# Kernel tuning notes

Measured on AMD Instinct MI355X. Metric: run time of the kernel, lower is better.

The kernel has to match this reference:

```python
import jax, jax.numpy as jnp
import numpy as np

NL, H, N, CIN, COUT, B, L = 4, 256, 64, 64, 8, 8, 1024
LN_EPS = 1e-5


def layernorm(x, w, b):
    m = x.mean(-1, keepdims=True)
    v = ((x - m) ** 2).mean(-1, keepdims=True)
    return (x - m) / jnp.sqrt(v + LN_EPS) * w + b


def s4d(u, A, C, D, log_step):
    # u: [B, H, L] real; A: [N] complex; C: [H, N] complex
    Lq = u.shape[-1]
    step = jnp.exp(log_step)                       # [H]
    dA = step[:, None] * A[None, :]                # [H, N] complex
    C_bar = C * (jnp.exp(dA) - 1.0) / A[None, :]   # [H, N]
    l = jnp.arange(Lq, dtype=jnp.float32)
    P = jnp.exp(l[:, None, None] * dA[None])       # [L, H, N] complex (dominant intermediate)
    K = jnp.einsum('hn,lhn->hl', C_bar, P)         # [H, L] complex
    kf = jnp.fft.rfft(K.real, n=2 * Lq) + 1j * jnp.fft.rfft(K.imag, n=2 * Lq)  # [H, L+1]
    uf = jnp.fft.rfft(u, n=2 * Lq)                 # [B, H, L+1]
    y = jnp.fft.irfft(kf * uf, n=2 * Lq)[..., :Lq]  # [B, H, L] real
    return y + u * D[:, None]


def forward(stimulus_seq, initial_state, A_re, A_im, C_re, C_im, D, log_step,
            ln1_w, ln1_b, ln2_w, ln2_b, W1, b1, W2, b2,
            Win, b_in, Wst, b_st, Wout, b_out):
    # stimulus_seq: [B, CIN, L] -> [B, L, CIN]
    x = stimulus_seq.transpose(0, 2, 1) @ Win.T + b_in            # [B, L, H]
    x = x + (initial_state @ Wst.T + b_st)[:, None, :]            # fusion_mode='add'
    for i in range(NL):
        xn = layernorm(x, ln1_w[i], ln1_b[i])
        A = A_re[i] + 1j * A_im[i]
        C = C_re[i] + 1j * C_im[i]
        y = s4d(xn.transpose(0, 2, 1), A, C, D[i], log_step[i])
        x = x + y.transpose(0, 2, 1)
        xn = layernorm(x, ln2_w[i], ln2_b[i])
        h = jax.nn.gelu(xn @ W1[i].T + b1[i], approximate=False)  # torch GELU = exact erf
        x = x + h @ W2[i].T + b2[i]
    out = x @ Wout.T + b_out                                      # [B, L, COUT]
    # use_voltage_filter=False: split + concat is identity on channel axis
    return out.transpose(0, 2, 1)                                 # [B, COUT, L]


def setup_inputs() -> dict:
    key = jax.random.key(0)
    ks = iter(jax.random.split(key, 24))
    def u(shape, fan_in):
        lim = 1.0 / np.sqrt(fan_in)
        return jax.random.uniform(next(ks), shape, minval=-lim, maxval=lim, dtype=jnp.float32)
    inp = {
        'stimulus_seq': jax.random.normal(next(ks), (B, CIN, L), dtype=jnp.float32),
        'initial_state': jax.random.normal(next(ks), (B, COUT), dtype=jnp.float32),
        'A_re': -0.5 * jnp.ones((NL, N), dtype=jnp.float32),
        'A_im': jnp.tile(jnp.arange(N, dtype=jnp.float32) * np.float32(np.pi), (NL, 1)),
        'C_re': jax.random.normal(next(ks), (NL, H, N), dtype=jnp.float32),
        'C_im': jax.random.normal(next(ks), (NL, H, N), dtype=jnp.float32),
        'D': jax.random.normal(next(ks), (NL, H), dtype=jnp.float32),
        'log_step': jax.random.uniform(next(ks), (NL, H), dtype=jnp.float32) * np.float32(np.log(0.1) - np.log(1e-4)) + np.float32(np.log(1e-4)),
        'ln1_w': jnp.ones((NL, H), dtype=jnp.float32),
        'ln1_b': jnp.zeros((NL, H), dtype=jnp.float32),
        'ln2_w': jnp.ones((NL, H), dtype=jnp.float32),
        'ln2_b': jnp.zeros((NL, H), dtype=jnp.float32),
        'W1': u((NL, 2 * H, H), H), 'b1': u((NL, 2 * H), H),
        'W2': u((NL, H, 2 * H), 2 * H), 'b2': u((NL, H), 2 * H),
        'Win': u((H, CIN), CIN), 'b_in': u((H,), CIN),
        'Wst': u((H, COUT), COUT), 'b_st': u((H,), COUT),
        'Wout': u((COUT, H), H), 'b_out': u((COUT,), H),
    }
    return inp


def reference(stimulus_seq, initial_state, A_re, A_im, C_re, C_im, D, log_step,
              ln1_w, ln1_b, ln2_w, ln2_b, W1, b1, W2, b2,
              Win, b_in, Wst, b_st, Wout, b_out):
    return forward(stimulus_seq, initial_state, A_re, A_im, C_re, C_im, D, log_step,
                   ln1_w, ln1_b, ln2_w, ln2_b, W1, b1, W2, b2,
                   Win, b_in, Wst, b_st, Wout, b_out)
```

## Files before the change

### kernel.cpp

```cpp
#include <hip/hip_runtime.h>
#include <math.h>

#define NL   4
#define H    256
#define NST  64
#define CIN  64
#define COUT 8
#define BB   8
#define LL   1024
#define NFFT 2048

typedef __attribute__((ext_vector_type(8))) short bf16x8;
typedef __attribute__((ext_vector_type(4))) short short4v;
typedef __attribute__((ext_vector_type(4))) int   int4v;
typedef __attribute__((ext_vector_type(4))) float f32x4;

__device__ __forceinline__ short f2bf(float f) {
  union { float f; unsigned u; } v; v.f = f;
  unsigned r = (v.u + 0x7fffu + ((v.u >> 16) & 1u)) >> 16;
  return (short)r;
}
__device__ __forceinline__ float b2f(short s) {
  union { unsigned u; float f; } v;
  v.u = ((unsigned)(unsigned short)s) << 16;
  return v.f;
}
__device__ __forceinline__ int IDX2(int a) { return a + (a >> 4); }
#define FBUF 2176

__device__ __forceinline__ float2 cadd(float2 a, float2 b) { return make_float2(a.x + b.x, a.y + b.y); }
__device__ __forceinline__ float2 csub(float2 a, float2 b) { return make_float2(a.x - b.x, a.y - b.y); }

template <int SGN>
__device__ __forceinline__ void bfly8(const float2 a[8], float2 A[8]) {
  const float RH = 0.70710678118654752f;
  float2 s0 = cadd(a[0], a[4]), s1 = csub(a[0], a[4]);
  float2 s2 = cadd(a[2], a[6]), s3 = csub(a[2], a[6]);
  float2 mi = (SGN < 0) ? make_float2(s3.y, -s3.x) : make_float2(-s3.y, s3.x);
  float2 E0 = cadd(s0, s2), E1 = cadd(s1, mi), E2 = csub(s0, s2), E3 = csub(s1, mi);
  float2 t0 = cadd(a[1], a[5]), t1 = csub(a[1], a[5]);
  float2 t2 = cadd(a[3], a[7]), t3 = csub(a[3], a[7]);
  float2 mj = (SGN < 0) ? make_float2(t3.y, -t3.x) : make_float2(-t3.y, t3.x);
  float2 O0 = cadd(t0, t2), O1 = cadd(t1, mj), O2 = csub(t0, t2), O3 = csub(t1, mj);
  float2 W0 = O0;
  float2 W1 = (SGN < 0) ? make_float2((O1.x + O1.y) * RH, (O1.y - O1.x) * RH)
                        : make_float2((O1.x - O1.y) * RH, (O1.x + O1.y) * RH);
  float2 W2 = (SGN < 0) ? make_float2(O2.y, -O2.x) : make_float2(-O2.y, O2.x);
  float2 W3 = (SGN < 0) ? make_float2((O3.y - O3.x) * RH, -(O3.x + O3.y) * RH)
                        : make_float2(-(O3.x + O3.y) * RH, (O3.x - O3.y) * RH);
  A[0] = cadd(E0, W0); A[4] = csub(E0, W0);
  A[1] = cadd(E1, W1); A[5] = csub(E1, W1);
  A[2] = cadd(E2, W2); A[6] = csub(E2, W2);
  A[3] = cadd(E3, W3); A[7] = csub(E3, W3);
}

template <int SGN>
__device__ __forceinline__ void fft_stage0_reg(const float2 a[8], float2* d,
                                               const float2* __restrict__ tw, int tid) {
  float2 A[8];
  bfly8<SGN>(a, A);
  const int base = 8 * tid;
  d[IDX2(base)] = A[0];
#pragma unroll
  for (int dd = 1; dd < 8; ++dd) {
    float2 w = tw[dd * tid];
    float wi = (SGN < 0) ? w.y : -w.y;
    d[IDX2(base + dd)] = make_float2(A[dd].x * w.x - A[dd].y * wi,
                                     A[dd].x * wi + A[dd].y * w.x);
  }
}

template <int SGN>
__device__ __forceinline__ void fft_stage0_reg_tw(const float2 a[8], float2* d,
                                                  const float2 w[7], int tid) {
  float2 A[8];
  bfly8<SGN>(a, A);
  const int base = 8 * tid;
  d[IDX2(base)] = A[0];
#pragma unroll
  for (int dd = 1; dd < 8; ++dd) {
    float wr = w[dd - 1].x;
    float wi = (SGN < 0) ? w[dd - 1].y : -w[dd - 1].y;
    d[IDX2(base + dd)] = make_float2(A[dd].x * wr - A[dd].y * wi,
                                     A[dd].x * wi + A[dd].y * wr);
  }
}

template <int SGN>
__device__ __forceinline__ void fft_mid_stages(float2* bA, float2* bB,
                                               const float2* __restrict__ tw, int tid) {
#pragma unroll
  for (int st = 1; st < 3; ++st) {
    float2* s = (st == 1) ? bA : bB;
    float2* d = (st == 1) ? bB : bA;
    const int m = 1 << (3 * st);
    __syncthreads();
    const int k  = tid & (m - 1);
    const int jm = tid - k;
    float2 a[8], A[8];
#pragma unroll
    for (int q = 0; q < 8; ++q) a[q] = s[IDX2(tid + 256 * q)];
    bfly8<SGN>(a, A);
    const int base = 8 * jm + k;
    d[IDX2(base)] = A[0];
#pragma unroll
    for (int dd = 1; dd < 8; ++dd) {
      float2 w = tw[dd * jm];
      float wi = (SGN < 0) ? w.y : -w.y;
      d[IDX2(base + dd * m)] = make_float2(A[dd].x * w.x - A[dd].y * wi,
                                           A[dd].x * wi + A[dd].y * w.x);
    }
  }
}

template <int SGN>
__device__ __forceinline__ void fft_final_r4_lds(const float2* s, float2* d, int tid) {
  __syncthreads();
#pragma unroll
  for (int q = 0; q < 2; ++q) {
    const int t = tid + (q << 8);
    float2 x0 = s[IDX2(t)], x1 = s[IDX2(t + 512)];
    float2 x2 = s[IDX2(t + 1024)], x3 = s[IDX2(t + 1536)];
    float2 s0 = cadd(x0, x2), s1 = csub(x0, x2);
    float2 s2 = cadd(x1, x3), s3 = csub(x1, x3);
    float2 mi = (SGN < 0) ? make_float2(s3.y, -s3.x) : make_float2(-s3.y, s3.x);
    d[IDX2(t)]        = cadd(s0, s2);
    d[IDX2(t + 512)]  = cadd(s1, mi);
    d[IDX2(t + 1024)] = csub(s0, s2);
    d[IDX2(t + 1536)] = csub(s1, mi);
  }
  __syncthreads();
}

template <int SGN>
__device__ __forceinline__ void fft_final_r4_reg(const float2* s, int tid,
                                                 float2 out0[4], float2 out1[4]) {
  __syncthreads();
#pragma unroll
  for (int q = 0; q < 2; ++q) {
    const int t = tid + (q << 8);
    float2 x0 = s[IDX2(t)], x1 = s[IDX2(t + 512)];
    float2 x2 = s[IDX2(t + 1024)], x3 = s[IDX2(t + 1536)];
    float2 s0 = cadd(x0, x2), s1 = csub(x0, x2);
    float2 s2 = cadd(x1, x3), s3 = csub(x1, x3);
    float2 mi = (SGN < 0) ? make_float2(s3.y, -s3.x) : make_float2(-s3.y, s3.x);
    float2* o = q ? out1 : out0;
    o[0] = cadd(s0, s2);
    o[1] = cadd(s1, mi);
    o[2] = csub(s0, s2);
    o[3] = csub(s1, mi);
  }
}

__global__ __launch_bounds__(256) void k_setup(
    const float* __restrict__ W1, const float* __restrict__ W2, const float* __restrict__ Win,
    const float* __restrict__ init, const float* __restrict__ Wst,
    const float* __restrict__ bst, const float* __restrict__ bin,
    short* __restrict__ W1s, short* __restrict__ W2s, float* __restrict__ WinT,
    float* __restrict__ sp, float2* __restrict__ tw) {
  int idx = blockIdx.x * 256 + threadIdx.x;
  if (idx < 2048) {
    float s, c;
    sincosf(3.14159265358979323846f * (float)idx / 1024.0f, &s, &c);
    tw[idx] = make_float2(c, -s);
  }
  if (idx < 65536) {
    int i = idx >> 14, c = idx & 16383;
    int cblk = c >> 11, s = (c >> 8) & 7, n = (c >> 6) & 3, lane = c & 63;
    int cl = lane & 15, rg = lane >> 4;
    int col = cblk * 64 + n * 16 + cl;
    const float* srcp = W1 + ((size_t)(i * 512 + col)) * 256 + s * 32 + rg * 8;
    short* dstp = W1s + ((size_t)idx) * 8;
#pragma unroll
    for (int j = 0; j < 8; ++j) dstp[j] = f2bf(srcp[j]);
  } else if (idx < 131072) {
    int t = idx - 65536;
    int i = t >> 14, c = t & 16383;
    int cblk = c >> 11, s = (c >> 7) & 15, n = (c >> 6) & 1, lane = c & 63;
    int cl = lane & 15, rg = lane >> 4;
    int col = cblk * 32 + n * 16 + cl;
    const float* srcp = W2 + ((size_t)(i * 256 + col)) * 512 + s * 32 + rg * 8;
    short* dstp = W2s + ((size_t)t) * 8;
#pragma unroll
    for (int j = 0; j < 8; ++j) dstp[j] = f2bf(srcp[j]);
  }
  if (idx < 256 * 64) {
    int hh = idx / 64, c = idx % 64;
    WinT[c * 256 + hh] = Win[idx];
  }
  if (idx < BB * H) {
    int b = idx >> 8, h = idx & 255;
    float acc = bin[h] + bst[h];
#pragma unroll
    for (int c = 0; c < COUT; ++c) acc += init[b * COUT + c] * Wst[h * COUT + c];
    sp[idx] = acc;
  }
}

__global__ __launch_bounds__(256) void k_in_ln1(
    const float* __restrict__ stim, const float* __restrict__ WinT,
    const float* __restrict__ sp, const float* __restrict__ lw, const float* __restrict__ lb,
    short* __restrict__ x, float* __restrict__ xnT) {
  int blk = blockIdx.x;
  int b_ = blk >> 6, l0 = (blk & 63) << 4;
  int tid = threadIdx.x, wv = tid >> 6, lane = tid & 63;
  __shared__ float sc[16][CIN];
  __shared__ float T[16][256];
#pragma unroll
  for (int it = 0; it < 4; ++it) {
    int idx = tid + (it << 8);
    int r = idx & 15, c = idx >> 4;
    sc[r][c] = stim[(b_ * CIN + c) * LL + l0 + r];
  }
  __syncthreads();
  float4 sp4 = *(const float4*)&sp[b_ * H + lane * 4];
  float4 acc[4] = {sp4, sp4, sp4, sp4};
  for (int c = 0; c < CIN; ++c) {
    float4 wv4 = *(const float4*)&WinT[c * H + lane * 4];
#pragma unroll
    for (int rr = 0; rr < 4; ++rr) {
      float s = sc[wv * 4 + rr][c];
      acc[rr].x += s * wv4.x; acc[rr].y += s * wv4.y;
      acc[rr].z += s * wv4.z; acc[rr].w += s * wv4.w;
    }
  }
  float4 w4 = *(const float4*)&lw[lane * 4];
  float4 c4 = *(const float4*)&lb[lane * 4];
#pragma unroll
  for (int rr = 0; rr < 4; ++rr) {
    int lr = wv * 4 + rr;
    float4 v = acc[rr];
    short4v s4;
    s4[0] = f2bf(v.x); s4[1] = f2bf(v.y); s4[2] = f2bf(v.z); s4[3] = f2bf(v.w);
    *(short4v*)&x[(((size_t)(b_ << 10) + l0 + lr)) * H + lane * 4] = s4;
    float s = v.x + v.y + v.z + v.w;
#pragma unroll
    for (int o = 32; o > 0; o >>= 1) s += __shfl_xor(s, o, 64);
    float m = s * (1.0f / H);
    float dx = v.x - m, dy = v.y - m, dz = v.z - m, dw = v.w - m;
    float q = dx * dx + dy * dy + dz * dz + dw * dw;
#pragma unroll
    for (int o = 32; o > 0; o >>= 1) q += __shfl_xor(q, o, 64);
    float rs = rsqrtf(q * (1.0f / H) + 1e-5f);
    float4 o4;
    o4.x = dx * rs * w4.x + c4.x; o4.y = dy * rs * w4.y + c4.y;
    o4.z = dz * rs * w4.z + c4.z; o4.w = dw * rs * w4.w + c4.w;
    *(float4*)&T[lr][lane * 4] = o4;
  }
  __syncthreads();
  float tmp[16];
#pragma unroll
  for (int l = 0; l < 16; ++l) tmp[l] = T[l][tid];
  float* dst = xnT + ((size_t)(b_ * H + tid)) * LL + l0;
#pragma unroll
  for (int l = 0; l < 16; l += 4) {
    float4 v = {tmp[l], tmp[l + 1], tmp[l + 2], tmp[l + 3]};
    *(float4*)&dst[l] = v;
  }
}

__global__ __launch_bounds__(256) void k_kernelfft(
    const float* __restrict__ A_re, const float* __restrict__ A_im,
    const float* __restrict__ C_re, const float* __restrict__ C_im,
    const float* __restrict__ log_step, const float2* __restrict__ tw,
    float2* __restrict__ kf) {
  int blk = blockIdx.x;
  int i = blk >> 8;
  int tid = threadIdx.x;
  __shared__ float2 cb[NST], Mv[NST];
  __shared__ float2 bufA[FBUF], bufB[FBUF];
  float2* T1 = bufB;
  float2* T2 = bufB + 1024;
  float step = expf(log_step[blk]);
  int n = tid & 63, g = tid >> 6;
  float Ar = A_re[i * NST + n], Ai = A_im[i * NST + n];
  float dr = step * Ar, di = step * Ai;
  float er = expf(dr);
  float sn, cs; sincosf(di, &sn, &cs);
  float Er = er * cs, Ei = er * sn;
  if (g == 0) {
    float nr = Er - 1.0f, ni = Ei;
    float dnm = Ar * Ar + Ai * Ai;
    float qr = (nr * Ar + ni * Ai) / dnm;
    float qi = (ni * Ar - nr * Ai) / dnm;
    float Cr = C_re[(size_t)blk * NST + n], Ci = C_im[(size_t)blk * NST + n];
    cb[n] = make_float2(Cr * qr - Ci * qi, Cr * qi + Ci * qr);
    float pr = 1.f, pi = 0.f;
    T1[n * 16] = make_float2(1.f, 0.f);
    for (int a = 1; a < 16; ++a) {
      float t2 = pr * Er - pi * Ei; pi = pr * Ei + pi * Er; pr = t2;
      T1[n * 16 + a] = make_float2(pr, pi);
    }
  } else if (g == 1) {
    float xr = Er, xi = Ei;
#pragma unroll
    for (int j = 0; j < 4; ++j) { float t2 = xr * xr - xi * xi; xi = 2.f * xr * xi; xr = t2; }
    float pr = 1.f, pi = 0.f;
    T2[n * 16] = make_float2(1.f, 0.f);
    for (int a = 1; a < 16; ++a) {
      float t2 = pr * xr - pi * xi; pi = pr * xi + pi * xr; pr = t2;
      T2[n * 16 + a] = make_float2(pr, pi);
    }
    float mr2 = pr * xr - pi * xi, mi2 = pr * xi + pi * xr;
    Mv[n] = make_float2(mr2, mi2);
  }
  __syncthreads();
  float kr[4] = {0.f, 0.f, 0.f, 0.f}, ki[4] = {0.f, 0.f, 0.f, 0.f};
  const int a_lo = tid & 15, a_hi = tid >> 4;
  for (int nn = 0; nn < NST; ++nn) {
    float2 t1 = T1[nn * 16 + a_lo];
    float2 t2v = T2[nn * 16 + a_hi];
    float pr = t1.x * t2v.x - t1.y * t2v.y;
    float pi = t1.x * t2v.y + t1.y * t2v.x;
    float2 c = cb[nn], m = Mv[nn];
#pragma unroll
    for (int q = 0; q < 4; ++q) {
      kr[q] += c.x * pr - c.y * pi;
      ki[q] += c.x * pi + c.y * pr;
      float t2 = pr * m.x - pi * m.y;
      pi = pr * m.y + pi * m.x;
      pr = t2;
    }
  }
  float2 a[8];
#pragma unroll
  for (int q = 0; q < 4; ++q) a[q] = make_float2(kr[q], ki[q]);
  a[4] = a[5] = a[6] = a[7] = make_float2(0.f, 0.f);
  fft_stage0_reg<-1>(a, bufA, tw, tid);
  fft_mid_stages<-1>(bufA, bufB, tw, tid);
  float2 F0[4], F1[4];
  fft_final_r4_reg<-1>(bufA, tid, F0, F1);
  float2* kfh = kf + (size_t)blk * 1025;
  kfh[tid]       = F0[0];
  kfh[tid + 512] = F0[1];
  kfh[tid + 256] = F1[0];
  kfh[tid + 768] = F1[1];
  if (tid == 0) kfh[1024] = F0[2];
}

__global__ __launch_bounds__(256) void k_conv(
    const float* __restrict__ xnT, const float2* __restrict__ kf,
    const float* __restrict__ D, const float2* __restrict__ tw, short* __restrict__ yT) {
  int blk = blockIdx.x;
  int b_ = blk >> 7, hp = blk & 127;
  int h0 = hp * 2, h1 = h0 + 1;
  int r0 = b_ * H + h0;
  int tid = threadIdx.x;
  __shared__ float2 bufA[FBUF], bufB[FBUF];
  float2 w0[7];
#pragma unroll
  for (int dd = 1; dd < 8; ++dd) w0[dd - 1] = tw[dd * tid];
  float u0[4], u1[4];
  const float* x0 = xnT + (size_t)r0 * LL;
  const float* x1 = x0 + LL;
  float2 a[8];
#pragma unroll
  for (int q = 0; q < 4; ++q) {
    int l = tid + (q << 8);
    float v0 = x0[l], v1 = x1[l];
    u0[q] = v0; u1[q] = v1;
    a[q] = make_float2(v0, v1);
  }
  a[4] = a[5] = a[6] = a[7] = make_float2(0.f, 0.f);
  fft_stage0_reg_tw<-1>(a, bufA, w0, tid);
  fft_mid_stages<-1>(bufA, bufB, tw, tid);
  fft_final_r4_lds<-1>(bufA, bufB, tid);
  const float2* kf0 = kf + (size_t)h0 * 1025;
  const float2* kf1 = kf + (size_t)h1 * 1025;
#pragma unroll
  for (int q = 0; q < 4; ++q) {
    int k = tid + (q << 8);
    if (k == 0) {
      float2 k0 = kf0[0], k1 = kf1[0];
      float2 F0 = bufB[IDX2(0)], Fn = bufB[IDX2(1024)];
      bufA[IDX2(0)]    = make_float2(F0.x * k0.x, F0.y * k1.x);
      float2 k0n = kf0[1024], k1n = kf1[1024];
      bufA[IDX2(1024)] = make_float2(Fn.x * k0n.x, Fn.y * k1n.x);
    } else {
      float2 F = bufB[IDX2(k)], G = bufB[IDX2(2048 - k)];
      float u0r = 0.5f * (F.x + G.x), u0i = 0.5f * (F.y - G.y);
      float dr_ = 0.5f * (F.x - G.x), di_ = 0.5f * (F.y + G.y);
      float u1r = di_, u1i = -dr_;
      float2 k0 = kf0[k], k1 = kf1[k];
      float z0r = u0r * k0.x - u0i * k0.y, z0i = u0r * k0.y + u0i * k0.x;
      float z1r = u1r * k1.x - u1i * k1.y, z1i = u1r * k1.y + u1i * k1.x;
      bufA[IDX2(k)]        = make_float2(z0r - z1i, z0i + z1r);
      bufA[IDX2(2048 - k)] = make_float2(z0r + z1i, z1r - z0i);
    }
  }
  __syncthreads();
  float2 g[8];
#pragma unroll
  for (int q = 0; q < 8; ++q) g[q] = bufA[IDX2(tid + 256 * q)];
  fft_stage0_reg_tw<1>(g, bufB, w0, tid);
  fft_mid_stages<1>(bufB, bufA, tw, tid);
  float2 z0[4], z1[4];
  fft_final_r4_reg<1>(bufB, tid, z0, z1);
  float Dh0 = D[h0], Dh1 = D[h1];
  short* y0 = yT + (size_t)r0 * LL;
  short* y1 = y0 + LL;
  const float s = 1.0f / NFFT;
  y0[tid]       = f2bf(z0[0].x * s + Dh0 * u0[0]);
  y0[tid + 256] = f2bf(z1[0].x * s + Dh0 * u0[1]);
  y0[tid + 512] = f2bf(z0[1].x * s + Dh0 * u0[2]);
  y0[tid + 768] = f2bf(z1[1].x * s + Dh0 * u0[3]);
  y1[tid]       = f2bf(z0[0].y * s + Dh1 * u1[0]);
  y1[tid + 256] = f2bf(z1[0].y * s + Dh1 * u1[1]);
  y1[tid + 512] = f2bf(z0[1].y * s + Dh1 * u1[2]);
  y1[tid + 768] = f2bf(z1[1].y * s + Dh1 * u1[3]);
}

#define TXS 260
template <bool LAST>
__global__ __launch_bounds__(512, 4) void k_mlp(
    const short* __restrict__ W1p, const float* __restrict__ b1p,
    const short* __restrict__ W2p, const float* __restrict__ b2p,
    short* __restrict__ x, const short* __restrict__ yT,
    const float* __restrict__ ln2w, const float* __restrict__ ln2b,
    const float* __restrict__ ln1w, const float* __restrict__ ln1b,
    float* __restrict__ xnT,
    const float* __restrict__ Wout, const float* __restrict__ bout,
    float* __restrict__ out) {
  const int m0 = blockIdx.x * 16;
  const int b_ = m0 >> 10, l0 = m0 & 1023;
  const int tid = threadIdx.x;
  const int lane = tid & 63, wid = tid >> 6;
  const int rg = lane >> 4, cl = lane & 15;
  __shared__ __attribute__((aligned(16))) char smem[26112];
  short* A1  = (short*)smem;
  short* A2  = (short*)(smem + 8448);
  float* red = (float*)(smem + 25088);
  float* Txn = (float*)smem;
  float* wlds = (float*)(smem + 16896);

  const short* w1base = W1p + (size_t)wid * 16384 + lane * 8;
  const short* w2base = W2p + (size_t)wid * 16384 + lane * 8;
  bf16x8 pre[8];
#pragma unroll
  for (int n = 0; n < 8; ++n)
    pre[n] = *(const bf16x8*)(w1base + n * 512);

  float v[2][4];
  float wl2[2], bl2[2];
#pragma unroll
  for (int n = 0; n < 2; ++n) {
    int col = wid * 32 + n * 16 + cl;
    wl2[n] = ln2w[col]; bl2[n] = ln2b[col];
  }
  float sum[4], sq[4];
#pragma unroll
  for (int r = 0; r < 4; ++r) { sum[r] = 0.f; sq[r] = 0.f; }
#pragma unroll
  for (int n = 0; n < 2; ++n) {
    int col = wid * 32 + n * 16 + cl;
    short4v y4 = *(const short4v*)&yT[((size_t)(b_ * H + col)) * LL + l0 + rg * 4];
    float yv[4] = {b2f(y4[0]), b2f(y4[1]), b2f(y4[2]), b2f(y4[3])};
#pragma unroll
    for (int r = 0; r < 4; ++r) {
      int row = rg * 4 + r;
      float val = b2f(x[(size_t)(m0 + row) * H + col]) + yv[r];
      v[n][r] = val;
      sum[r] += val; sq[r] += val * val;
    }
  }
#pragma unroll
  for (int r = 0; r < 4; ++r) {
#pragma unroll
    for (int o = 1; o < 16; o <<= 1) {
      sum[r] += __shfl_xor(sum[r], o, 64);
      sq[r]  += __shfl_xor(sq[r], o, 64);
    }
  }
  if (cl == 0) {
#pragma unroll
    for (int r = 0; r < 4; ++r) {
      int row = rg * 4 + r;
      red[(wid * 16 + row) * 2]     = sum[r];
      red[(wid * 16 + row) * 2 + 1] = sq[r];
    }
  }
  __syncthreads();
#pragma unroll
  for (int r = 0; r < 4; ++r) {
    int row = rg * 4 + r;
    float S = 0.f, Q = 0.f;
#pragma unroll
    for (int w = 0; w < 8; ++w) { S += red[(w * 16 + row) * 2]; Q += red[(w * 16 + row) * 2 + 1]; }
    float mean = S * (1.0f / H);
    float var = Q * (1.0f / H) - mean * mean;
    float rs = rsqrtf(var + 1e-5f);
#pragma unroll
    for (int n = 0; n < 2; ++n) {
      int col = wid * 32 + n * 16 + cl;
      A1[row * 264 + col] = f2bf((v[n][r] - mean) * rs * wl2[n] + bl2[n]);
    }
  }
  __syncthreads();

  f32x4 acc1[4];
#pragma unroll
  for (int n = 0; n < 4; ++n) acc1[n] = (f32x4){0.f, 0.f, 0.f, 0.f};
  {
#pragma unroll
    for (int s = 0; s < 8; ++s) {
      const int kk = s * 32;
      bf16x8 af, bfv[4];
      if (s < 2) {
#pragma unroll
        for (int n = 0; n < 4; ++n) bfv[n] = pre[s * 4 + n];
      } else {
#pragma unroll
        for (int n = 0; n < 4; ++n)
          bfv[n] = *(const bf16x8*)(w1base + (s * 4 + n) * 512);
      }
      af = *(const bf16x8*)&A1[cl * 264 + kk + rg * 8];
      __builtin_amdgcn_s_setprio(1);
#pragma unroll
      for (int n = 0; n < 4; ++n)
        acc1[n] = __builtin_amdgcn_mfma_f32_16x16x32_bf16(af, bfv[n], acc1[n], 0, 0, 0);
      __builtin_amdgcn_s_setprio(0);
    }
  }
  bf16x8 pre2[4];
#pragma unroll
  for (int n = 0; n < 4; ++n)
    pre2[n] = *(const bf16x8*)(w2base + n * 512);
#pragma unroll
  for (int n = 0; n < 4; ++n) {
    int col = wid * 64 + n * 16 + cl;
    float bb = b1p[col];
#pragma unroll
    for (int r = 0; r < 4; ++r) {
      int row = rg * 4 + r;
      float g = acc1[n][r] + bb;
      g = 0.5f * g * (1.0f + erff(g * 0.70710678118654752f));
      A2[row * 520 + col] = f2bf(g);
    }
  }
  __syncthreads();

  f32x4 acc2[2];
#pragma unroll
  for (int n = 0; n < 2; ++n) acc2[n] = (f32x4){0.f, 0.f, 0.f, 0.f};
  {
#pragma unroll
    for (int s = 0; s < 16; ++s) {
      const int kk = s * 32;
      bf16x8 af, bfv[2];
      if (s < 2) {
#pragma unroll
        for (int n = 0; n < 2; ++n) bfv[n] = pre2[s * 2 + n];
      } else {
#pragma unroll
        for (int n = 0; n < 2; ++n)
          bfv[n] = *(const bf16x8*)(w2base + (s * 2 + n) * 512);
      }
      af = *(const bf16x8*)&A2[cl * 520 + kk + rg * 8];
      __builtin_amdgcn_s_setprio(1);
#pragma unroll
      for (int n = 0; n < 2; ++n)
        acc2[n] = __builtin_amdgcn_mfma_f32_16x16x32_bf16(af, bfv[n], acc2[n], 0, 0, 0);
      __builtin_amdgcn_s_setprio(0);
    }
  }

  float bv[2], wl1[2], bl1[2];
#pragma unroll
  for (int n = 0; n < 2; ++n) {
    int col = wid * 32 + n * 16 + cl;
    bv[n] = b2p[col];
    if (!LAST) { wl1[n] = ln1w[col]; bl1[n] = ln1b[col]; }
  }
#pragma unroll
  for (int r = 0; r < 4; ++r) { sum[r] = 0.f; sq[r] = 0.f; }
#pragma unroll
  for (int n = 0; n < 2; ++n) {
#pragma unroll
    for (int r = 0; r < 4; ++r) {
      float vf = acc2[n][r] + bv[n] + v[n][r];
      acc2[n][r] = vf;
      sum[r] += vf; sq[r] += vf * vf;
    }
  }

  if (LAST) {
    __syncthreads();
#pragma unroll
    for (int n = 0; n < 2; ++n) {
      int col = wid * 32 + n * 16 + cl;
#pragma unroll
      for (int r = 0; r < 4; ++r) {
        int row = rg * 4 + r;
        Txn[row * TXS + col] = acc2[n][r];
      }
    }
#pragma unroll
    for (int it = 0; it < 4; ++it) {
      int idx = tid + (it << 9);
      wlds[(idx >> 8) * 258 + (idx & 255)] = Wout[idx];
    }
    __syncthreads();
    if (tid < 128) {
      int row = tid >> 3, co = tid & 7;
      float p = bout[co];
      const float* tr = Txn + row * TXS;
      const float* wr = wlds + co * 258;
#pragma unroll 4
      for (int c = 0; c < H; ++c) p += tr[c] * wr[c];
      out[((b_ * COUT + co) << 10) + l0 + row] = p;
    }
  } else {
#pragma unroll
    for (int r = 0; r < 4; ++r) {
#pragma unroll
      for (int o = 1; o < 16; o <<= 1) {
        sum[r] += __shfl_xor(sum[r], o, 64);
        sq[r]  += __shfl_xor(sq[r], o, 64);
      }
    }
    if (cl == 0) {
#pragma unroll
      for (int r = 0; r < 4; ++r) {
        int row = rg * 4 + r;
        red[(wid * 16 + row) * 2]     = sum[r];
        red[(wid * 16 + row) * 2 + 1] = sq[r];
      }
    }
    __syncthreads();
#pragma unroll
    for (int r = 0; r < 4; ++r) {
      int row = rg * 4 + r;
      float S = 0.f, Q = 0.f;
#pragma unroll
      for (int w = 0; w < 8; ++w) { S += red[(w * 16 + row) * 2]; Q += red[(w * 16 + row) * 2 + 1]; }
      float mean = S * (1.0f / H);
      float var = Q * (1.0f / H) - mean * mean;
      float rs = rsqrtf(var + 1e-5f);
#pragma unroll
      for (int n = 0; n < 2; ++n) {
        int col = wid * 32 + n * 16 + cl;
        float vf = acc2[n][r];
        x[(size_t)(m0 + row) * H + col] = f2bf(vf);
        Txn[row * TXS + col] = (vf - mean) * rs * wl1[n] + bl1[n];
      }
    }
    __syncthreads();
    int h = tid & 255, seg = (tid >> 8) * 8;
    float tmp[8];
#pragma unroll
    for (int l = 0; l < 8; ++l) tmp[l] = Txn[(seg + l) * TXS + h];
    float* dst = xnT + ((size_t)(b_ * H + h)) * LL + l0 + seg;
#pragma unroll
    for (int l = 0; l < 8; l += 4) {
      float4 v4 = {tmp[l], tmp[l + 1], tmp[l + 2], tmp[l + 3]};
      *(float4*)&dst[l] = v4;
    }
  }
}

extern "C" void kernel_launch(void* const* d_in, const int* in_sizes, int n_in,
                              void* d_out, int out_size, void* d_ws, size_t ws_size,
                              hipStream_t stream) {
  const float* stim  = (const float*)d_in[0];
  const float* init  = (const float*)d_in[1];
  const float* A_re  = (const float*)d_in[2];
  const float* A_im  = (const float*)d_in[3];
  const float* C_re  = (const float*)d_in[4];
  const float* C_im  = (const float*)d_in[5];
  const float* Dp    = (const float*)d_in[6];
  const float* lstep = (const float*)d_in[7];
  const float* ln1w  = (const float*)d_in[8];
  const float* ln1b  = (const float*)d_in[9];
  const float* ln2w  = (const float*)d_in[10];
  const float* ln2b  = (const float*)d_in[11];
  const float* W1    = (const float*)d_in[12];
  const float* b1    = (const float*)d_in[13];
  const float* W2    = (const float*)d_in[14];
  const float* b2    = (const float*)d_in[15];
  const float* Win   = (const float*)d_in[16];
  const float* bin   = (const float*)d_in[17];
  const float* Wst   = (const float*)d_in[18];
  const float* bst   = (const float*)d_in[19];
  const float* Wout  = (const float*)d_in[20];
  const float* bout  = (const float*)d_in[21];
  float* out = (float*)d_out;
  float* ws = (float*)d_ws;

  size_t o = 0;
  auto alloc = [&](size_t nfloats) { size_t r = o; o += (nfloats + 63) & ~(size_t)63; return r; };
  short*  x    = (short*)(ws + alloc((size_t)BB * LL * H / 2));
  float*  xnT  = ws + alloc((size_t)BB * H * LL);
  short*  yT   = (short*)(ws + alloc((size_t)BB * H * LL / 2));
  float2* kf   = (float2*)(ws + alloc((size_t)NL * H * 1025 * 2));
  short*  W1s  = (short*)(ws + alloc((size_t)NL * 512 * 256 / 2));
  short*  W2s  = (short*)(ws + alloc((size_t)NL * 256 * 512 / 2));
  float*  WinT = ws + alloc((size_t)64 * 256);
  float*  sp   = ws + alloc((size_t)BB * H);
  float2* tw   = (float2*)(ws + alloc((size_t)2048 * 2));
  (void)ws_size; (void)in_sizes; (void)n_in; (void)out_size;

  k_setup<<<512, 256, 0, stream>>>(W1, W2, Win, init, Wst, bst, bin,
                                   W1s, W2s, WinT, sp, tw);
  k_kernelfft<<<NL * H, 256, 0, stream>>>(A_re, A_im, C_re, C_im, lstep, tw, kf);
  k_in_ln1<<<BB * 64, 256, 0, stream>>>(stim, WinT, sp, ln1w, ln1b, x, xnT);

  for (int i = 0; i < NL; ++i) {
    k_conv<<<BB * H / 2, 256, 0, stream>>>(xnT, kf + (size_t)i * H * 1025,
                                           Dp + i * H, tw, yT);
    if (i < NL - 1) {
      k_mlp<false><<<512, 512, 0, stream>>>(
          W1s + (size_t)i * 512 * 256, b1 + i * 512,
          W2s + (size_t)i * 256 * 512, b2 + i * H,
          x, yT, ln2w + i * H, ln2b + i * H,
          ln1w + (i + 1) * H, ln1b + (i + 1) * H, xnT,
          nullptr, nullptr, nullptr);
    } else {
      k_mlp<true><<<512, 512, 0, stream>>>(
          W1s + (size_t)i * 512 * 256, b1 + i * 512,
          W2s + (size_t)i * 256 * 512, b2 + i * H,
          x, yT, ln2w + i * H, ln2b + i * H,
          nullptr, nullptr, nullptr,
          Wout, bout, out);
    }
  }
}
```

Measured before the change: 175.9 us.

## Store residual stream transposed and fuse spectral multiply into inverse FFT registers

The bf16 residual x is now stored in [B,H,L] layout, matching yT, so the MLP kernel reads and writes it with short4 vector accesses along L instead of scattered 2-byte accesses. The input kernel transposes through LDS to write the new layout. Separately, the conv kernel computes the spectral product directly into registers for the inverse FFT stage 0, dropping an LDS write, a barrier and a reload. The cost is an extra LDS transpose pass with two barriers in k_in_ln1, and some duplicated loads in the conv kernel.

```diff
diff --git a/kernel.cpp b/kernel.cpp
--- a/kernel.cpp
+++ b/kernel.cpp
@@ -200,7 +200,7 @@
 __global__ __launch_bounds__(256) void k_in_ln1(
     const float* __restrict__ stim, const float* __restrict__ WinT,
     const float* __restrict__ sp, const float* __restrict__ lw, const float* __restrict__ lb,
-    short* __restrict__ x, float* __restrict__ xnT) {
+    short* __restrict__ xT, float* __restrict__ xnT) {
   int blk = blockIdx.x;
   int b_ = blk >> 6, l0 = (blk & 63) << 4;
   int tid = threadIdx.x, wv = tid >> 6, lane = tid & 63;
@@ -224,15 +224,27 @@
       acc[rr].z += s * wv4.z; acc[rr].w += s * wv4.w;
     }
   }
+#pragma unroll
+  for (int rr = 0; rr < 4; ++rr)
+    *(float4*)&T[wv * 4 + rr][lane * 4] = acc[rr];
+  __syncthreads();
+  {
+    bf16x8 v0, v1;
+#pragma unroll
+    for (int l = 0; l < 8; ++l) v0[l] = f2bf(T[l][tid]);
+#pragma unroll
+    for (int l = 0; l < 8; ++l) v1[l] = f2bf(T[l + 8][tid]);
+    short* dst = xT + ((size_t)(b_ * H + tid)) * LL + l0;
+    *(bf16x8*)&dst[0] = v0;
+    *(bf16x8*)&dst[8] = v1;
+  }
+  __syncthreads();
   float4 w4 = *(const float4*)&lw[lane * 4];
   float4 c4 = *(const float4*)&lb[lane * 4];
 #pragma unroll
   for (int rr = 0; rr < 4; ++rr) {
     int lr = wv * 4 + rr;
     float4 v = acc[rr];
-    short4v s4;
-    s4[0] = f2bf(v.x); s4[1] = f2bf(v.y); s4[2] = f2bf(v.z); s4[3] = f2bf(v.w);
-    *(short4v*)&x[(((size_t)(b_ << 10) + l0 + lr)) * H + lane * 4] = s4;
     float s = v.x + v.y + v.z + v.w;
 #pragma unroll
     for (int o = 32; o > 0; o >>= 1) s += __shfl_xor(s, o, 64);
@@ -367,35 +379,36 @@
   fft_final_r4_lds<-1>(bufA, bufB, tid);
   const float2* kf0 = kf + (size_t)h0 * 1025;
   const float2* kf1 = kf + (size_t)h1 * 1025;
-#pragma unroll
-  for (int q = 0; q < 4; ++q) {
+  float2 g[8];
+#pragma unroll
+  for (int q = 0; q < 8; ++q) {
     int k = tid + (q << 8);
-    if (k == 0) {
-      float2 k0 = kf0[0], k1 = kf1[0];
-      float2 F0 = bufB[IDX2(0)], Fn = bufB[IDX2(1024)];
-      bufA[IDX2(0)]    = make_float2(F0.x * k0.x, F0.y * k1.x);
-      float2 k0n = kf0[1024], k1n = kf1[1024];
-      bufA[IDX2(1024)] = make_float2(Fn.x * k0n.x, Fn.y * k1n.x);
+    float2 Z;
+    if (tid == 0 && q == 0) {
+      float2 Fz = bufB[IDX2(0)];
+      Z = make_float2(Fz.x * kf0[0].x, Fz.y * kf1[0].x);
+    } else if (tid == 0 && q == 4) {
+      float2 Fn = bufB[IDX2(1024)];
+      Z = make_float2(Fn.x * kf0[1024].x, Fn.y * kf1[1024].x);
     } else {
-      float2 F = bufB[IDX2(k)], G = bufB[IDX2(2048 - k)];
-      float u0r = 0.5f * (F.x + G.x), u0i = 0.5f * (F.y - G.y);
-      float dr_ = 0.5f * (F.x - G.x), di_ = 0.5f * (F.y + G.y);
+      int km = (k < 1024) ? k : 2048 - k;
+      float2 Flo = bufB[IDX2(km)];
+      float2 Fhi = bufB[IDX2(2048 - km)];
+      float u0r = 0.5f * (Flo.x + Fhi.x), u0i = 0.5f * (Flo.y - Fhi.y);
+      float dr_ = 0.5f * (Flo.x - Fhi.x), di_ = 0.5f * (Flo.y + Fhi.y);
       float u1r = di_, u1i = -dr_;
-      float2 k0 = kf0[k], k1 = kf1[k];
+      float2 k0 = kf0[km], k1 = kf1[km];
       float z0r = u0r * k0.x - u0i * k0.y, z0i = u0r * k0.y + u0i * k0.x;
       float z1r = u1r * k1.x - u1i * k1.y, z1i = u1r * k1.y + u1i * k1.x;
-      bufA[IDX2(k)]        = make_float2(z0r - z1i, z0i + z1r);
-      bufA[IDX2(2048 - k)] = make_float2(z0r + z1i, z1r - z0i);
-    }
-  }
-  __syncthreads();
-  float2 g[8];
-#pragma unroll
-  for (int q = 0; q < 8; ++q) g[q] = bufA[IDX2(tid + 256 * q)];
-  fft_stage0_reg_tw<1>(g, bufB, w0, tid);
-  fft_mid_stages<1>(bufB, bufA, tw, tid);
+      Z = (k < 1024) ? make_float2(z0r - z1i, z0i + z1r)
+                     : make_float2(z0r + z1i, z1r - z0i);
+    }
+    g[q] = Z;
+  }
+  fft_stage0_reg_tw<1>(g, bufA, w0, tid);
+  fft_mid_stages<1>(bufA, bufB, tw, tid);
   float2 z0[4], z1[4];
-  fft_final_r4_reg<1>(bufB, tid, z0, z1);
+  fft_final_r4_reg<1>(bufA, tid, z0, z1);
   float Dh0 = D[h0], Dh1 = D[h1];
   short* y0 = yT + (size_t)r0 * LL;
   short* y1 = y0 + LL;
@@ -415,7 +428,7 @@
 __global__ __launch_bounds__(512, 4) void k_mlp(
     const short* __restrict__ W1p, const float* __restrict__ b1p,
     const short* __restrict__ W2p, const float* __restrict__ b2p,
-    short* __restrict__ x, const short* __restrict__ yT,
+    short* __restrict__ xT, const short* __restrict__ yT,
     const float* __restrict__ ln2w, const float* __restrict__ ln2b,
     const float* __restrict__ ln1w, const float* __restrict__ ln1b,
     float* __restrict__ xnT,
@@ -453,12 +466,12 @@
 #pragma unroll
   for (int n = 0; n < 2; ++n) {
     int col = wid * 32 + n * 16 + cl;
-    short4v y4 = *(const short4v*)&yT[((size_t)(b_ * H + col)) * LL + l0 + rg * 4];
-    float yv[4] = {b2f(y4[0]), b2f(y4[1]), b2f(y4[2]), b2f(y4[3])};
+    size_t base = ((size_t)(b_ * H + col)) * LL + l0 + rg * 4;
+    short4v y4 = *(const short4v*)&yT[base];
+    short4v x4 = *(const short4v*)&xT[base];
 #pragma unroll
     for (int r = 0; r < 4; ++r) {
-      int row = rg * 4 + r;
-      float val = b2f(x[(size_t)(m0 + row) * H + col]) + yv[r];
+      float val = b2f(x4[r]) + b2f(y4[r]);
       v[n][r] = val;
       sum[r] += val; sq[r] += val * val;
     }
@@ -627,6 +640,7 @@
       }
     }
     __syncthreads();
+    short4v xs[2];
 #pragma unroll
     for (int r = 0; r < 4; ++r) {
       int row = rg * 4 + r;
@@ -640,9 +654,14 @@
       for (int n = 0; n < 2; ++n) {
         int col = wid * 32 + n * 16 + cl;
         float vf = acc2[n][r];
-        x[(size_t)(m0 + row) * H + col] = f2bf(vf);
+        xs[n][r] = f2bf(vf);
         Txn[row * TXS + col] = (vf - mean) * rs * wl1[n] + bl1[n];
       }
+    }
+#pragma unroll
+    for (int n = 0; n < 2; ++n) {
+      int col = wid * 32 + n * 16 + cl;
+      *(short4v*)&xT[((size_t)(b_ * H + col)) * LL + l0 + rg * 4] = xs[n];
     }
     __syncthreads();
     int h = tid & 255, seg = (tid >> 8) * 8;
@@ -688,7 +707,7 @@
 
   size_t o = 0;
   auto alloc = [&](size_t nfloats) { size_t r = o; o += (nfloats + 63) & ~(size_t)63; return r; };
-  short*  x    = (short*)(ws + alloc((size_t)BB * LL * H / 2));
+  short*  xT   = (short*)(ws + alloc((size_t)BB * LL * H / 2));
   float*  xnT  = ws + alloc((size_t)BB * H * LL);
   short*  yT   = (short*)(ws + alloc((size_t)BB * H * LL / 2));
   float2* kf   = (float2*)(ws + alloc((size_t)NL * H * 1025 * 2));
@@ -702,7 +721,7 @@
   k_setup<<<512, 256, 0, stream>>>(W1, W2, Win, init, Wst, bst, bin,
                                    W1s, W2s, WinT, sp, tw);
   k_kernelfft<<<NL * H, 256, 0, stream>>>(A_re, A_im, C_re, C_im, lstep, tw, kf);
-  k_in_ln1<<<BB * 64, 256, 0, stream>>>(stim, WinT, sp, ln1w, ln1b, x, xnT);
+  k_in_ln1<<<BB * 64, 256, 0, stream>>>(stim, WinT, sp, ln1w, ln1b, xT, xnT);
 
   for (int i = 0; i < NL; ++i) {
     k_conv<<<BB * H / 2, 256, 0, stream>>>(xnT, kf + (size_t)i * H * 1025,
@@ -711,14 +730,14 @@
       k_mlp<false><<<512, 512, 0, stream>>>(
           W1s + (size_t)i * 512 * 256, b1 + i * 512,
           W2s + (size_t)i * 256 * 512, b2 + i * H,
-          x, yT, ln2w + i * H, ln2b + i * H,
+          xT, yT, ln2w + i * H, ln2b + i * H,
           ln1w + (i + 1) * H, ln1b + (i + 1) * H, xnT,
           nullptr, nullptr, nullptr);
     } else {
       k_mlp<true><<<512, 512, 0, stream>>>(
           W1s + (size_t)i * 512 * 256, b1 + i * 512,
           W2s + (size_t)i * 256 * 512, b2 + i * H,
-          x, yT, ln2w + i * H, ln2b + i * H,
+          xT, yT, ln2w + i * H, ln2b + i * H,
           nullptr, nullptr, nullptr,
           Wout, bout, out);
     }
```

New measurement: 188.6 us. 7.2% more time.
